# Kernel tuning notes

Hardware: AMD Instinct MI355X
Metric: run time of the kernel (lower is better)

## Reference

```python
import jax, jax.numpy as jnp
import numpy as np

N_NODES = 50000
N_EDGES = 800000
NFEAT, NHID, NOUT = 256, 256, 128


def setup_inputs() -> dict:
    key = jax.random.key(0)
    ks = jax.random.split(key, 5)
    stdv1 = 1.0 / np.sqrt(NHID)
    stdv2 = 1.0 / np.sqrt(NOUT)
    x = jax.random.normal(ks[0], (N_NODES, NFEAT), dtype=jnp.float32)
    w1 = jax.random.uniform(ks[1], (NFEAT, NHID), minval=-stdv1, maxval=stdv1, dtype=jnp.float32)
    w2 = jax.random.uniform(ks[2], (NHID, NOUT), minval=-stdv2, maxval=stdv2, dtype=jnp.float32)
    edge_src = jax.random.randint(ks[3], (N_EDGES,), 0, N_NODES, dtype=jnp.int32)
    edge_dst = jax.random.randint(ks[4], (N_EDGES,), 0, N_NODES, dtype=jnp.int32)
    return {"x": x, "w1": w1, "w2": w2, "edge_src": edge_src, "edge_dst": edge_dst}


def _gcn_layer(h, w, edge_src, edge_dst, n):
    # support = h @ w ; out[i] = sum_{(src,dst=i) in E} support[src]  (SpMM with 0/1 adj)
    support = jnp.dot(h, w)                      # [N, out]
    return jax.ops.segment_sum(support[edge_src], edge_dst, num_segments=n)


def reference(x, w1, w2, edge_src, edge_dst):
    n = x.shape[0]
    h = jax.nn.relu(_gcn_layer(x, w1, edge_src, edge_dst, n))
    # dropout is identity in eval mode (training=False)
    out = _gcn_layer(h, w2, edge_src, edge_dst, n)
    return out
```

## Files before the change

### kernel.cpp

```cpp
#include <hip/hip_runtime.h>
#include <hip/hip_bf16.h>


#define NFEAT 256
#define NOUT  128
#define CHUNK 4096
#define P4CAP 5120

typedef short short8 __attribute__((ext_vector_type(8)));
typedef float floatx4 __attribute__((ext_vector_type(4)));
typedef float floatx2 __attribute__((ext_vector_type(2)));

typedef const __attribute__((address_space(1))) unsigned short GAS_US;
typedef __attribute__((address_space(3))) unsigned short LAS_US;

__device__ __forceinline__ unsigned short f2bf(float f) {
    unsigned u = __builtin_bit_cast(unsigned, f);
    unsigned r = (u + 0x7FFFu + ((u >> 16) & 1u)) >> 16;
    return (unsigned short)r;
}
__device__ __forceinline__ unsigned char f2fp8(float f) {
    int p = __builtin_amdgcn_cvt_pk_fp8_f32(f, f, 0, false);
    return (unsigned char)(p & 0xFF);
}
__device__ __forceinline__ void accf8(float* a, uint2 v) {
    floatx2 f0 = __builtin_amdgcn_cvt_pk_f32_fp8(v.x, false);
    floatx2 f1 = __builtin_amdgcn_cvt_pk_f32_fp8(v.x, true);
    floatx2 f2 = __builtin_amdgcn_cvt_pk_f32_fp8(v.y, false);
    floatx2 f3 = __builtin_amdgcn_cvt_pk_f32_fp8(v.y, true);
    a[0] += f0.x; a[1] += f0.y; a[2] += f1.x; a[3] += f1.y;
    a[4] += f2.x; a[5] += f2.y; a[6] += f3.x; a[7] += f3.y;
}


__global__ __launch_bounds__(256) void k_prep(const float* __restrict__ w1,
                                              const float* __restrict__ w2,
                                              unsigned short* __restrict__ w1T,
                                              unsigned short* __restrict__ w2T,
                                              const int* __restrict__ edst,
                                              int* __restrict__ counts_bm,
                                              int E, int bins, int pblk) {
    __shared__ int h[256];
    int b = blockIdx.x, tid = threadIdx.x;
    if (b < 256) {
        int idx = b * 256 + tid;
        int nn = idx >> 8, k = idx & 255;
        w1T[idx] = f2bf(w1[k * 256 + nn]);
        return;
    }
    if (b < 384) {
        int idx = (b - 256) * 256 + tid;
        int nn = idx >> 8, k = idx & 255;
        w2T[idx] = f2bf(w2[k * 128 + nn]);
        return;
    }
    int blk = b - 384;
    h[tid] = 0;
    __syncthreads();
    int base = blk * CHUNK;
#pragma unroll
    for (int t = 0; t < CHUNK / 256; ++t) {
        int i = base + t * 256 + tid;
        if (i < E) atomicAdd(&h[edst[i] >> 8], 1);
    }
    __syncthreads();
    for (int j = tid; j < bins; j += 256)
        counts_bm[j * pblk + blk] = h[j];
}


__global__ __launch_bounds__(1024) void k_scan1(const int* __restrict__ deg,
                                                int* __restrict__ excl,
                                                int* __restrict__ partials, int n) {
    __shared__ int s[1024];
    int gid = blockIdx.x * 1024 + threadIdx.x;
    int v = (gid < n) ? deg[gid] : 0;
    s[threadIdx.x] = v;
    __syncthreads();
    for (int off = 1; off < 1024; off <<= 1) {
        int t = (threadIdx.x >= off) ? s[threadIdx.x - off] : 0;
        __syncthreads();
        s[threadIdx.x] += t;
        __syncthreads();
    }
    if (gid < n) excl[gid] = s[threadIdx.x] - v;
    if (threadIdx.x == 1023) partials[blockIdx.x] = s[1023];
}

__global__ __launch_bounds__(1024) void k_scan3(int* __restrict__ excl,
                                                const int* __restrict__ partials,
                                                int n, int total) {
    __shared__ int pfx;
    if (threadIdx.x < 64) {
        int v = ((int)threadIdx.x < (int)blockIdx.x) ? partials[threadIdx.x] : 0;
        for (int o = 32; o > 0; o >>= 1) v += __shfl_down(v, o, 64);
        if (threadIdx.x == 0) pfx = v;
    }
    __syncthreads();
    int gid = blockIdx.x * 1024 + threadIdx.x;
    if (gid < n) excl[gid] += pfx;
    if (gid == 0) excl[n] = total;
}


#define GBM 128
#define GBN 128
#define GBK 64

__global__ __launch_bounds__(256) void k_gemm1_scatter(
        const float* __restrict__ x,
        const unsigned short* __restrict__ BT,
        unsigned char* __restrict__ C,
        const int* __restrict__ esrc, const int* __restrict__ edst,
        const int* __restrict__ offs_bm,
        unsigned int* __restrict__ edgePk,
        int M, int E, int nGemm, int bins, int pblk) {
    __shared__ unsigned short As[GBM * GBK];
    __shared__ unsigned short Bs[GBN * GBK];
    int b = blockIdx.x, tid = threadIdx.x;

    if (b >= nGemm) {
        int blk = b - nGemm;
        int* baseOff = (int*)As;
        int* cur     = (int*)Bs;
        for (int j = tid; j < bins; j += 256) {
            baseOff[j] = offs_bm[j * pblk + blk];
            cur[j] = 0;
        }
        __syncthreads();
        int base = blk * CHUNK;
#pragma unroll
        for (int t = 0; t < CHUNK / 256; ++t) {
            int i = base + t * 256 + tid;
            if (i < E) {
                int d = edst[i], s = esrc[i];
                int bin = d >> 8;
                int pos = atomicAdd(&cur[bin], 1);
                edgePk[baseOff[bin] + pos] = ((unsigned)d << 16) | (unsigned)s;
            }
        }
        return;
    }

    const int N = 256, K = 256;
    int bx = b >> 1, by = b & 1;
    int lane = tid & 63, wave = tid >> 6;
    int wm = (wave >> 1) * 64, wn = (wave & 1) * 64;
    int q = lane >> 4, r = lane & 15;
    int m0 = bx * GBM, n0 = by * GBN;
    int srow = (lane >> 3);
    int scol = (lane & 7) * 8;

    floatx4 acc[4][4];
#pragma unroll
    for (int i = 0; i < 4; ++i)
#pragma unroll
        for (int j = 0; j < 4; ++j) acc[i][j] = (floatx4){0.f, 0.f, 0.f, 0.f};

    for (int k0 = 0; k0 < K; k0 += GBK) {
#pragma unroll
        for (int t = 0; t < 4; ++t) {
            int row = wave * 32 + t * 8 + srow;
            __builtin_amdgcn_global_load_lds(
                (GAS_US*)&BT[(size_t)(n0 + row) * K + k0 + scol],
                (LAS_US*)&Bs[(wave * 32 + t * 8) * GBK], 16, 0, 0);
        }
#pragma unroll
        for (int u = 0; u < 4; ++u) {
            int unit = tid + u * 256;
            int row = unit >> 3, cg = unit & 7;
            int gm = m0 + row; if (gm >= M) gm = M - 1;
            const float* src = &x[(size_t)gm * 256 + k0 + cg * 8];
            float4 f0 = *(const float4*)src;
            float4 f1 = *(const float4*)(src + 4);
            short8 v;
            v[0] = (short)f2bf(f0.x); v[1] = (short)f2bf(f0.y);
            v[2] = (short)f2bf(f0.z); v[3] = (short)f2bf(f0.w);
            v[4] = (short)f2bf(f1.x); v[5] = (short)f2bf(f1.y);
            v[6] = (short)f2bf(f1.z); v[7] = (short)f2bf(f1.w);
            *(short8*)&As[row * GBK + cg * 8] = v;
        }
        __syncthreads();
#pragma unroll
        for (int kk = 0; kk < GBK; kk += 32) {
            short8 af[4], bfr[4];
#pragma unroll
            for (int i = 0; i < 4; ++i)
                af[i] = *(const short8*)&As[(wm + i * 16 + r) * GBK + kk + q * 8];
#pragma unroll
            for (int j = 0; j < 4; ++j)
                bfr[j] = *(const short8*)&Bs[(wn + j * 16 + r) * GBK + kk + q * 8];
#pragma unroll
            for (int i = 0; i < 4; ++i)
#pragma unroll
                for (int j = 0; j < 4; ++j)
                    acc[i][j] = __builtin_amdgcn_mfma_f32_16x16x32_bf16(
                        af[i], bfr[j], acc[i][j], 0, 0, 0);
        }
        __syncthreads();
    }

#pragma unroll
    for (int i = 0; i < 4; ++i) {
#pragma unroll
        for (int rr = 0; rr < 4; ++rr) {
            int grow = m0 + wm + i * 16 + q * 4 + rr;
            if (grow < M) {
                size_t base = (size_t)grow * N + n0 + wn;
#pragma unroll
                for (int j = 0; j < 4; ++j)
                    C[base + j * 16 + r] = f2fp8(acc[i][j][rr]);
            }
        }
    }
}


__global__ __launch_bounds__(256) void k_p4(const unsigned int* __restrict__ edgePk,
                                            const int* __restrict__ offs_bm,
                                            unsigned short* __restrict__ csr,
                                            int* __restrict__ offsets,
                                            int N, int E, int bins, int pblk) {
    __shared__ unsigned int buf[P4CAP];
    __shared__ int h[256], loff[256], cur[256];
    int b = blockIdx.x, tid = threadIdx.x;
    int s0 = offs_bm[b * pblk];
    int s1 = (b + 1 < bins) ? offs_bm[(b + 1) * pblk] : E;
    int n = s1 - s0; if (n > P4CAP) n = P4CAP;
    h[tid] = 0;
    __syncthreads();
    for (int i = tid; i < n; i += 256) {
        unsigned int p = edgePk[s0 + i];
        buf[i] = p;
        atomicAdd(&h[(p >> 16) & 255], 1);
    }
    __syncthreads();
    int v = h[tid];
    loff[tid] = v;
    __syncthreads();
    for (int off = 1; off < 256; off <<= 1) {
        int t2 = (tid >= off) ? loff[tid - off] : 0;
        __syncthreads();
        loff[tid] += t2;
        __syncthreads();
    }
    int excl = loff[tid] - v;
    int node = b * 256 + tid;
    if (node < N) offsets[node] = s0 + excl;
    if (b == bins - 1 && tid == 0) offsets[N] = E;
    cur[tid] = 0;
    __syncthreads();
    loff[tid] = excl;
    __syncthreads();
    for (int i = tid; i < n; i += 256) {
        unsigned int p = buf[i];
        int ld = (p >> 16) & 255;
        int pos = atomicAdd(&cur[ld], 1);
        csr[s0 + loff[ld] + pos] = (unsigned short)(p & 0xFFFFu);
    }
}


__global__ __launch_bounds__(256) void k_gemm2(const unsigned short* __restrict__ A,
                                               const unsigned short* __restrict__ BT,
                                               unsigned char* __restrict__ C,
                                               int M, int N, int K) {
    __shared__ unsigned short As[GBM * GBK];
    __shared__ unsigned short Bs[GBN * GBK];
    int tid = threadIdx.x;
    int lane = tid & 63, wave = tid >> 6;
    int wm = (wave >> 1) * 64, wn = (wave & 1) * 64;
    int q = lane >> 4, r = lane & 15;
    int m0 = blockIdx.x * GBM, n0 = blockIdx.y * GBN;
    int srow = (lane >> 3);
    int scol = (lane & 7) * 8;

    floatx4 acc[4][4];
#pragma unroll
    for (int i = 0; i < 4; ++i)
#pragma unroll
        for (int j = 0; j < 4; ++j) acc[i][j] = (floatx4){0.f, 0.f, 0.f, 0.f};

    for (int k0 = 0; k0 < K; k0 += GBK) {
#pragma unroll
        for (int t = 0; t < 4; ++t) {
            int row = wave * 32 + t * 8 + srow;
            int gm = m0 + row; if (gm >= M) gm = M - 1;
            __builtin_amdgcn_global_load_lds(
                (GAS_US*)&A[(size_t)gm * K + k0 + scol],
                (LAS_US*)&As[(wave * 32 + t * 8) * GBK], 16, 0, 0);
            __builtin_amdgcn_global_load_lds(
                (GAS_US*)&BT[(size_t)(n0 + row) * K + k0 + scol],
                (LAS_US*)&Bs[(wave * 32 + t * 8) * GBK], 16, 0, 0);
        }
        __syncthreads();
#pragma unroll
        for (int kk = 0; kk < GBK; kk += 32) {
            short8 af[4], bfr[4];
#pragma unroll
            for (int i = 0; i < 4; ++i)
                af[i] = *(const short8*)&As[(wm + i * 16 + r) * GBK + kk + q * 8];
#pragma unroll
            for (int j = 0; j < 4; ++j)
                bfr[j] = *(const short8*)&Bs[(wn + j * 16 + r) * GBK + kk + q * 8];
#pragma unroll
            for (int i = 0; i < 4; ++i)
#pragma unroll
                for (int j = 0; j < 4; ++j)
                    acc[i][j] = __builtin_amdgcn_mfma_f32_16x16x32_bf16(
                        af[i], bfr[j], acc[i][j], 0, 0, 0);
        }
        __syncthreads();
    }

#pragma unroll
    for (int i = 0; i < 4; ++i) {
#pragma unroll
        for (int rr = 0; rr < 4; ++rr) {
            int grow = m0 + wm + i * 16 + q * 4 + rr;
            if (grow < M) {
                size_t base = (size_t)grow * N + n0 + wn;
#pragma unroll
                for (int j = 0; j < 4; ++j)
                    C[base + j * 16 + r] = f2fp8(acc[i][j][rr]);
            }
        }
    }
}


__global__ __launch_bounds__(256) void k_gather_relu256(const unsigned char* __restrict__ sup,
                                                        const int* __restrict__ offsets,
                                                        const unsigned short* __restrict__ csr,
                                                        unsigned short* __restrict__ h, int n) {
    int lane = threadIdx.x & 63, wave = threadIdx.x >> 6;
    int half = lane >> 5, l32 = lane & 31;
    int node = blockIdx.x * 8 + wave * 2 + half;
    bool valid = node < n;
    int beg = valid ? offsets[node] : 0;
    int end = valid ? offsets[node + 1] : 0;
    int cnt = end - beg;
    const unsigned short* slot = &csr[beg];
    float a[8] = {};
    int e = 0;
    for (; e + 8 <= cnt; e += 8) {
        int s[8];
#pragma unroll
        for (int t = 0; t < 8; ++t) s[t] = slot[e + t];
        uint2 v[8];
#pragma unroll
        for (int t = 0; t < 8; ++t)
            v[t] = *(const uint2*)&sup[(size_t)s[t] * 256 + l32 * 8];
#pragma unroll
        for (int t = 0; t < 8; ++t) accf8(a, v[t]);
    }
    for (; e + 4 <= cnt; e += 4) {
        int s0 = slot[e], s1 = slot[e + 1], s2 = slot[e + 2], s3 = slot[e + 3];
        uint2 v0 = *(const uint2*)&sup[(size_t)s0 * 256 + l32 * 8];
        uint2 v1 = *(const uint2*)&sup[(size_t)s1 * 256 + l32 * 8];
        uint2 v2 = *(const uint2*)&sup[(size_t)s2 * 256 + l32 * 8];
        uint2 v3 = *(const uint2*)&sup[(size_t)s3 * 256 + l32 * 8];
        accf8(a, v0); accf8(a, v1); accf8(a, v2); accf8(a, v3);
    }
    for (; e < cnt; ++e) {
        uint2 v = *(const uint2*)&sup[(size_t)slot[e] * 256 + l32 * 8];
        accf8(a, v);
    }
    if (valid) {
        uint4 o;
        o.x = (unsigned)f2bf(fmaxf(a[0], 0.f)) | ((unsigned)f2bf(fmaxf(a[1], 0.f)) << 16);
        o.y = (unsigned)f2bf(fmaxf(a[2], 0.f)) | ((unsigned)f2bf(fmaxf(a[3], 0.f)) << 16);
        o.z = (unsigned)f2bf(fmaxf(a[4], 0.f)) | ((unsigned)f2bf(fmaxf(a[5], 0.f)) << 16);
        o.w = (unsigned)f2bf(fmaxf(a[6], 0.f)) | ((unsigned)f2bf(fmaxf(a[7], 0.f)) << 16);
        *(uint4*)&h[(size_t)node * 256 + l32 * 8] = o;
    }
}


__global__ __launch_bounds__(256) void k_gather128(const unsigned char* __restrict__ sup,
                                                   const int* __restrict__ offsets,
                                                   const unsigned short* __restrict__ csr,
                                                   float* __restrict__ outp, int n) {
    int lane = threadIdx.x & 63, wave = threadIdx.x >> 6;
    int quarter = lane >> 4, l16 = lane & 15;
    int node = blockIdx.x * 16 + wave * 4 + quarter;
    bool valid = node < n;
    int beg = valid ? offsets[node] : 0;
    int end = valid ? offsets[node + 1] : 0;
    int cnt = end - beg;
    const unsigned short* slot = &csr[beg];
    float a[8] = {};
    int e = 0;
    for (; e + 8 <= cnt; e += 8) {
        int s[8];
#pragma unroll
        for (int t = 0; t < 8; ++t) s[t] = slot[e + t];
        uint2 v[8];
#pragma unroll
        for (int t = 0; t < 8; ++t)
            v[t] = *(const uint2*)&sup[(size_t)s[t] * 128 + l16 * 8];
#pragma unroll
        for (int t = 0; t < 8; ++t) accf8(a, v[t]);
    }
    for (; e + 4 <= cnt; e += 4) {
        int s0 = slot[e], s1 = slot[e + 1], s2 = slot[e + 2], s3 = slot[e + 3];
        uint2 v0 = *(const uint2*)&sup[(size_t)s0 * 128 + l16 * 8];
        uint2 v1 = *(const uint2*)&sup[(size_t)s1 * 128 + l16 * 8];
        uint2 v2 = *(const uint2*)&sup[(size_t)s2 * 128 + l16 * 8];
        uint2 v3 = *(const uint2*)&sup[(size_t)s3 * 128 + l16 * 8];
        accf8(a, v0); accf8(a, v1); accf8(a, v2); accf8(a, v3);
    }
    for (; e < cnt; ++e) {
        uint2 v = *(const uint2*)&sup[(size_t)slot[e] * 128 + l16 * 8];
        accf8(a, v);
    }
    if (valid) {
        size_t base = (size_t)node * 128 + l16 * 8;
        *(float4*)&outp[base]     = make_float4(a[0], a[1], a[2], a[3]);
        *(float4*)&outp[base + 4] = make_float4(a[4], a[5], a[6], a[7]);
    }
}


extern "C" void kernel_launch(void* const* d_in, const int* in_sizes, int n_in,
                              void* d_out, int out_size, void* d_ws, size_t ws_size,
                              hipStream_t stream) {
    const float* x    = (const float*)d_in[0];
    const float* w1   = (const float*)d_in[1];
    const float* w2   = (const float*)d_in[2];
    const int*   esrc = (const int*)d_in[3];
    const int*   edst = (const int*)d_in[4];
    float*       out  = (float*)d_out;

    const int N = in_sizes[0] / NFEAT;
    const int E = in_sizes[3];

    const int bins = (N + 255) / 256;
    const int pblk = (E + CHUNK - 1) / CHUNK;
    const int nFlat = bins * pblk;

    char* ws = (char*)d_ws;
    size_t off = 0;
    unsigned short* hb   = (unsigned short*)(ws + off); off += (size_t)N * 256 * 2;
    unsigned char*  sup1 = (unsigned char*)(ws + off);  off += (size_t)N * 256;
    unsigned char*  sup2 = (unsigned char*)(ws + off);  off += (size_t)N * 128;
    unsigned short* w1T  = (unsigned short*)(ws + off); off += (size_t)256 * 256 * 2;
    unsigned short* w2T  = (unsigned short*)(ws + off); off += (size_t)128 * 256 * 2;
    off = (off + 255) & ~(size_t)255;
    int* counts_bm = (int*)(ws + off); off += (size_t)nFlat * sizeof(int);
    off = (off + 255) & ~(size_t)255;
    int* offs_bm   = (int*)(ws + off); off += ((size_t)nFlat + 1) * sizeof(int);
    off = (off + 255) & ~(size_t)255;
    int* partials  = (int*)(ws + off); off += 64 * sizeof(int);
    off = (off + 255) & ~(size_t)255;
    unsigned int* edgePk = (unsigned int*)(ws + off); off += (size_t)E * sizeof(unsigned int);
    off = (off + 255) & ~(size_t)255;
    unsigned short* csr  = (unsigned short*)(ws + off); off += (size_t)E * sizeof(unsigned short);
    off = (off + 255) & ~(size_t)255;
    int* offsets   = (int*)(ws + off); off += ((size_t)N + 1) * sizeof(int);
    (void)ws_size; (void)n_in; (void)out_size;

    k_prep<<<384 + pblk, 256, 0, stream>>>(w1, w2, w1T, w2T, edst, counts_bm,
                                           E, bins, pblk);

    int nb = (nFlat + 1023) / 1024;
    k_scan1<<<nb, 1024, 0, stream>>>(counts_bm, offs_bm, partials, nFlat);
    k_scan3<<<nb, 1024, 0, stream>>>(offs_bm, partials, nFlat, E);

    {
        int nGemm = 2 * ((N + GBM - 1) / GBM);
        k_gemm1_scatter<<<nGemm + pblk, 256, 0, stream>>>(
            x, w1T, sup1, esrc, edst, offs_bm, edgePk, N, E, nGemm, bins, pblk);
    }

    k_p4<<<bins, 256, 0, stream>>>(edgePk, offs_bm, csr, offsets, N, E, bins, pblk);

    k_gather_relu256<<<(N + 7) / 8, 256, 0, stream>>>(sup1, offsets, csr, hb, N);

    {
        dim3 grid((N + GBM - 1) / GBM, 128 / GBN);
        k_gemm2<<<grid, 256, 0, stream>>>(hb, w2T, sup2, N, 128, 256);
    }

    k_gather128<<<(N + 15) / 16, 256, 0, stream>>>(sup2, offsets, csr, out, N);
}
```

Baseline: 196.5 us.

## Restructure gather kernels to split edges across lanes and merge scan kernels

The two gather kernels now assign 8 lanes to edges and 8 lanes to features, so each wave processes 8 nodes in sequence. The feature dimension is split across blocks (quarters or halves) and partial sums are combined with cross-lane shuffle reductions. This is meant to expose more memory-level parallelism per node than the old one-node-per-half-wave layout with serial edge loops, at the cost of shuffle reductions and less coalesced 64-byte row slices. The two-pass prefix scan is also replaced by a single-block kernel, removing one launch and the partials buffer.

```diff
diff --git a/kernel.cpp b/kernel.cpp
--- a/kernel.cpp
+++ b/kernel.cpp
@@ -69,37 +69,31 @@
 }
 
 
-__global__ __launch_bounds__(1024) void k_scan1(const int* __restrict__ deg,
-                                                int* __restrict__ excl,
-                                                int* __restrict__ partials, int n) {
+__global__ __launch_bounds__(1024) void k_scan(const int* __restrict__ cnts,
+                                               int* __restrict__ excl,
+                                               int n, int per, int total) {
     __shared__ int s[1024];
-    int gid = blockIdx.x * 1024 + threadIdx.x;
-    int v = (gid < n) ? deg[gid] : 0;
-    s[threadIdx.x] = v;
+    int tid = threadIdx.x;
+    int base = tid * per;
+    int sum = 0;
+    for (int i = 0; i < per; ++i) {
+        int idx = base + i;
+        if (idx < n) sum += cnts[idx];
+    }
+    s[tid] = sum;
     __syncthreads();
     for (int off = 1; off < 1024; off <<= 1) {
-        int t = (threadIdx.x >= off) ? s[threadIdx.x - off] : 0;
-        __syncthreads();
-        s[threadIdx.x] += t;
-        __syncthreads();
-    }
-    if (gid < n) excl[gid] = s[threadIdx.x] - v;
-    if (threadIdx.x == 1023) partials[blockIdx.x] = s[1023];
-}
-
-__global__ __launch_bounds__(1024) void k_scan3(int* __restrict__ excl,
-                                                const int* __restrict__ partials,
-                                                int n, int total) {
-    __shared__ int pfx;
-    if (threadIdx.x < 64) {
-        int v = ((int)threadIdx.x < (int)blockIdx.x) ? partials[threadIdx.x] : 0;
-        for (int o = 32; o > 0; o >>= 1) v += __shfl_down(v, o, 64);
-        if (threadIdx.x == 0) pfx = v;
-    }
-    __syncthreads();
-    int gid = blockIdx.x * 1024 + threadIdx.x;
-    if (gid < n) excl[gid] += pfx;
-    if (gid == 0) excl[n] = total;
+        int t = (tid >= off) ? s[tid - off] : 0;
+        __syncthreads();
+        s[tid] += t;
+        __syncthreads();
+    }
+    int run = s[tid] - sum;
+    for (int i = 0; i < per; ++i) {
+        int idx = base + i;
+        if (idx < n) { int v = cnts[idx]; excl[idx] = run; run += v; }
+    }
+    if (tid == 1023) excl[n] = total;
 }
 
 
@@ -333,46 +327,35 @@
                                                         const int* __restrict__ offsets,
                                                         const unsigned short* __restrict__ csr,
                                                         unsigned short* __restrict__ h, int n) {
+    int qtr = blockIdx.x & 3;
+    int chunk = blockIdx.x >> 2;
     int lane = threadIdx.x & 63, wave = threadIdx.x >> 6;
-    int half = lane >> 5, l32 = lane & 31;
-    int node = blockIdx.x * 8 + wave * 2 + half;
-    bool valid = node < n;
-    int beg = valid ? offsets[node] : 0;
-    int end = valid ? offsets[node + 1] : 0;
-    int cnt = end - beg;
-    const unsigned short* slot = &csr[beg];
-    float a[8] = {};
-    int e = 0;
-    for (; e + 8 <= cnt; e += 8) {
-        int s[8];
-#pragma unroll
-        for (int t = 0; t < 8; ++t) s[t] = slot[e + t];
-        uint2 v[8];
-#pragma unroll
-        for (int t = 0; t < 8; ++t)
-            v[t] = *(const uint2*)&sup[(size_t)s[t] * 256 + l32 * 8];
-#pragma unroll
-        for (int t = 0; t < 8; ++t) accf8(a, v[t]);
-    }
-    for (; e + 4 <= cnt; e += 4) {
-        int s0 = slot[e], s1 = slot[e + 1], s2 = slot[e + 2], s3 = slot[e + 3];
-        uint2 v0 = *(const uint2*)&sup[(size_t)s0 * 256 + l32 * 8];
-        uint2 v1 = *(const uint2*)&sup[(size_t)s1 * 256 + l32 * 8];
-        uint2 v2 = *(const uint2*)&sup[(size_t)s2 * 256 + l32 * 8];
-        uint2 v3 = *(const uint2*)&sup[(size_t)s3 * 256 + l32 * 8];
-        accf8(a, v0); accf8(a, v1); accf8(a, v2); accf8(a, v3);
-    }
-    for (; e < cnt; ++e) {
-        uint2 v = *(const uint2*)&sup[(size_t)slot[e] * 256 + l32 * 8];
-        accf8(a, v);
-    }
-    if (valid) {
-        uint4 o;
-        o.x = (unsigned)f2bf(fmaxf(a[0], 0.f)) | ((unsigned)f2bf(fmaxf(a[1], 0.f)) << 16);
-        o.y = (unsigned)f2bf(fmaxf(a[2], 0.f)) | ((unsigned)f2bf(fmaxf(a[3], 0.f)) << 16);
-        o.z = (unsigned)f2bf(fmaxf(a[4], 0.f)) | ((unsigned)f2bf(fmaxf(a[5], 0.f)) << 16);
-        o.w = (unsigned)f2bf(fmaxf(a[6], 0.f)) | ((unsigned)f2bf(fmaxf(a[7], 0.f)) << 16);
-        *(uint4*)&h[(size_t)node * 256 + l32 * 8] = o;
+    int e8 = lane >> 3;
+    int fl = lane & 7;
+    int nodeBase = chunk * 32 + wave * 8;
+#pragma unroll
+    for (int i = 0; i < 8; ++i) {
+        int node = nodeBase + i;
+        if (node >= n) break;
+        int beg = offsets[node], end = offsets[node + 1];
+        float a[8] = {};
+        for (int e = beg + e8; e < end; e += 8) {
+            int s = csr[e];
+            uint2 v = *(const uint2*)&sup[(size_t)s * 256 + qtr * 64 + fl * 8];
+            accf8(a, v);
+        }
+#pragma unroll
+        for (int o = 8; o < 64; o <<= 1)
+#pragma unroll
+            for (int j = 0; j < 8; ++j) a[j] += __shfl_down(a[j], o, 64);
+        if (e8 == 0) {
+            uint4 ov;
+            ov.x = (unsigned)f2bf(fmaxf(a[0], 0.f)) | ((unsigned)f2bf(fmaxf(a[1], 0.f)) << 16);
+            ov.y = (unsigned)f2bf(fmaxf(a[2], 0.f)) | ((unsigned)f2bf(fmaxf(a[3], 0.f)) << 16);
+            ov.z = (unsigned)f2bf(fmaxf(a[4], 0.f)) | ((unsigned)f2bf(fmaxf(a[5], 0.f)) << 16);
+            ov.w = (unsigned)f2bf(fmaxf(a[6], 0.f)) | ((unsigned)f2bf(fmaxf(a[7], 0.f)) << 16);
+            *(uint4*)&h[(size_t)node * 256 + qtr * 64 + fl * 8] = ov;
+        }
     }
 }
 
@@ -381,43 +364,32 @@
                                                    const int* __restrict__ offsets,
                                                    const unsigned short* __restrict__ csr,
                                                    float* __restrict__ outp, int n) {
+    int hx = blockIdx.x & 1;
+    int chunk = blockIdx.x >> 1;
     int lane = threadIdx.x & 63, wave = threadIdx.x >> 6;
-    int quarter = lane >> 4, l16 = lane & 15;
-    int node = blockIdx.x * 16 + wave * 4 + quarter;
-    bool valid = node < n;
-    int beg = valid ? offsets[node] : 0;
-    int end = valid ? offsets[node + 1] : 0;
-    int cnt = end - beg;
-    const unsigned short* slot = &csr[beg];
-    float a[8] = {};
-    int e = 0;
-    for (; e + 8 <= cnt; e += 8) {
-        int s[8];
-#pragma unroll
-        for (int t = 0; t < 8; ++t) s[t] = slot[e + t];
-        uint2 v[8];
-#pragma unroll
-        for (int t = 0; t < 8; ++t)
-            v[t] = *(const uint2*)&sup[(size_t)s[t] * 128 + l16 * 8];
-#pragma unroll
-        for (int t = 0; t < 8; ++t) accf8(a, v[t]);
-    }
-    for (; e + 4 <= cnt; e += 4) {
-        int s0 = slot[e], s1 = slot[e + 1], s2 = slot[e + 2], s3 = slot[e + 3];
-        uint2 v0 = *(const uint2*)&sup[(size_t)s0 * 128 + l16 * 8];
-        uint2 v1 = *(const uint2*)&sup[(size_t)s1 * 128 + l16 * 8];
-        uint2 v2 = *(const uint2*)&sup[(size_t)s2 * 128 + l16 * 8];
-        uint2 v3 = *(const uint2*)&sup[(size_t)s3 * 128 + l16 * 8];
-        accf8(a, v0); accf8(a, v1); accf8(a, v2); accf8(a, v3);
-    }
-    for (; e < cnt; ++e) {
-        uint2 v = *(const uint2*)&sup[(size_t)slot[e] * 128 + l16 * 8];
-        accf8(a, v);
-    }
-    if (valid) {
-        size_t base = (size_t)node * 128 + l16 * 8;
-        *(float4*)&outp[base]     = make_float4(a[0], a[1], a[2], a[3]);
-        *(float4*)&outp[base + 4] = make_float4(a[4], a[5], a[6], a[7]);
+    int e8 = lane >> 3;
+    int fl = lane & 7;
+    int nodeBase = chunk * 32 + wave * 8;
+#pragma unroll
+    for (int i = 0; i < 8; ++i) {
+        int node = nodeBase + i;
+        if (node >= n) break;
+        int beg = offsets[node], end = offsets[node + 1];
+        float a[8] = {};
+        for (int e = beg + e8; e < end; e += 8) {
+            int s = csr[e];
+            uint2 v = *(const uint2*)&sup[(size_t)s * 128 + hx * 64 + fl * 8];
+            accf8(a, v);
+        }
+#pragma unroll
+        for (int o = 8; o < 64; o <<= 1)
+#pragma unroll
+            for (int j = 0; j < 8; ++j) a[j] += __shfl_down(a[j], o, 64);
+        if (e8 == 0) {
+            size_t base = (size_t)node * 128 + hx * 64 + fl * 8;
+            *(float4*)&outp[base]     = make_float4(a[0], a[1], a[2], a[3]);
+            *(float4*)&outp[base + 4] = make_float4(a[4], a[5], a[6], a[7]);
+        }
     }
 }
 
@@ -451,8 +423,6 @@
     off = (off + 255) & ~(size_t)255;
     int* offs_bm   = (int*)(ws + off); off += ((size_t)nFlat + 1) * sizeof(int);
     off = (off + 255) & ~(size_t)255;
-    int* partials  = (int*)(ws + off); off += 64 * sizeof(int);
-    off = (off + 255) & ~(size_t)255;
     unsigned int* edgePk = (unsigned int*)(ws + off); off += (size_t)E * sizeof(unsigned int);
     off = (off + 255) & ~(size_t)255;
     unsigned short* csr  = (unsigned short*)(ws + off); off += (size_t)E * sizeof(unsigned short);
@@ -463,9 +433,10 @@
     k_prep<<<384 + pblk, 256, 0, stream>>>(w1, w2, w1T, w2T, edst, counts_bm,
                                            E, bins, pblk);
 
-    int nb = (nFlat + 1023) / 1024;
-    k_scan1<<<nb, 1024, 0, stream>>>(counts_bm, offs_bm, partials, nFlat);
-    k_scan3<<<nb, 1024, 0, stream>>>(offs_bm, partials, nFlat, E);
+    {
+        int per = (nFlat + 1023) / 1024;
+        k_scan<<<1, 1024, 0, stream>>>(counts_bm, offs_bm, nFlat, per, E);
+    }
 
     {
         int nGemm = 2 * ((N + GBM - 1) / GBM);
@@ -475,12 +446,18 @@
 
     k_p4<<<bins, 256, 0, stream>>>(edgePk, offs_bm, csr, offsets, N, E, bins, pblk);
 
-    k_gather_relu256<<<(N + 7) / 8, 256, 0, stream>>>(sup1, offsets, csr, hb, N);
+    {
+        int nChunks = (N + 31) / 32;
+        k_gather_relu256<<<nChunks * 4, 256, 0, stream>>>(sup1, offsets, csr, hb, N);
+    }
 
     {
         dim3 grid((N + GBM - 1) / GBM, 128 / GBN);
         k_gemm2<<<grid, 256, 0, stream>>>(hb, w2T, sup2, N, 128, 256);
     }
 
-    k_gather128<<<(N + 15) / 16, 256, 0, stream>>>(sup2, offsets, csr, out, N);
-}
+    {
+        int nChunks = (N + 31) / 32;
+        k_gather128<<<nChunks * 2, 256, 0, stream>>>(sup2, offsets, csr, out, N);
+    }
+}
```

Result: slower. 320.8 us (+63.3%).
